# Kernel tuning notes

Hardware: AMD Instinct MI355X
Metric: run time of the kernel (lower is better)

## Reference

```python
import jax, jax.numpy as jnp
import numpy as np

# DeltaNet single-token decode step. Hard-coded dims from the torch source:
# hidden H=2048 (chosen), qk=2048 (16h x 128 -> repeat to 32h), v=4096 (32h x 128),
# conv channels 8192, kernel 4, state [1,32,128,128].
H = 2048
EPS = 1e-6

def _l2norm(x):
    return x * jax.lax.rsqrt(jnp.sum(x * x, axis=-1, keepdims=True) + EPS)

def setup_inputs() -> dict:
    key = jax.random.key(0)
    ks = jax.random.split(key, 12)
    w = lambda k, s, sc=0.02: jax.random.normal(k, s, dtype=jnp.float32) * sc
    return {
        "x": jax.random.normal(ks[0], (1, 1, H), dtype=jnp.float32),
        "state": jax.random.normal(ks[1], (1, 32, 128, 128), dtype=jnp.float32) * 0.02,
        "conv_state": jax.random.normal(ks[2], (1, 8192, 3), dtype=jnp.float32) * 0.1,
        "W_qkv": w(ks[3], (8192, H)),
        "W_z": w(ks[4], (4096, H)),
        "W_b": w(ks[5], (32, H)),
        "W_a": w(ks[6], (32, H)),
        "conv_w": w(ks[7], (8192, 1, 4), 0.3),
        "A_log": jax.random.uniform(ks[8], (32,), minval=-2.0, maxval=0.0, dtype=jnp.float32),
        "dt_bias": w(ks[9], (32,), 0.5),
        "norm_w": jnp.ones((128,), jnp.float32),
        "W_out": w(ks[10], (H, 4096)),
    }

def reference(x, state, conv_state, W_qkv, W_z, W_b, W_a, conv_w, A_log, dt_bias, norm_w, W_out):
    # projections (bias-free Linear, torch convention y = x @ W.T)
    mixed = jnp.einsum('blh,ch->blc', x, W_qkv)           # [1,1,8192]
    z = jnp.einsum('blh,ch->blc', x, W_z).reshape(1, 1, 32, 128)
    beta = jax.nn.sigmoid(jnp.einsum('blh,ch->blc', x, W_b))  # [1,1,32]
    a = jnp.einsum('blh,ch->blc', x, W_a)                 # [1,1,32]

    # depthwise causal conv (groups=8192, kernel 4, output length 1)
    combined = jnp.concatenate([conv_state, mixed.transpose(0, 2, 1)], axis=-1)  # [1,8192,4]
    new_conv = combined[:, :, -3:]
    conv_out = jnp.sum(combined * conv_w[None, :, 0, :], axis=-1)  # [1,8192]
    mixed = jax.nn.silu(conv_out)[:, None, :]             # [1,1,8192]

    q, k, v = mixed[..., :2048], mixed[..., 2048:4096], mixed[..., 4096:]
    q = jnp.repeat(q.reshape(1, 1, 16, 128), 2, axis=2)   # [1,1,32,128]
    k = jnp.repeat(k.reshape(1, 1, 16, 128), 2, axis=2)
    v = v.reshape(1, 1, 32, 128)

    g = -jnp.exp(A_log) * jax.nn.softplus(a + dt_bias)    # [1,1,32]

    q = _l2norm(q)[:, 0] / jnp.sqrt(jnp.float32(128.0))   # [1,32,128]
    k = _l2norm(k)[:, 0]
    v = v[:, 0]
    g_t = jnp.exp(g[:, 0])[..., None, None]               # [1,32,1,1]
    beta_t = beta[:, 0][..., None]                        # [1,32,1]

    # gated delta-rule state update
    s = state * g_t                                       # [1,32,128,128]
    kv_mem = jnp.einsum('bhkv,bhk->bhv', s, k)            # [1,32,128]
    delta = (v - kv_mem) * beta_t
    new_state = s + k[..., None] * delta[..., None, :]    # [1,32,128,128]
    out = jnp.einsum('bhkv,bhk->bhv', new_state, q)       # [1,32,128]

    # gated RMSNorm (Mamba2-style: rmsnorm(x * silu(z)) * w)
    out_flat = out.reshape(-1, 128)
    z_flat = z.reshape(-1, 128)
    gated = out_flat * jax.nn.silu(z_flat)
    out_flat = gated * jax.lax.rsqrt(jnp.mean(gated * gated, axis=-1, keepdims=True) + EPS) * norm_w

    out = jnp.einsum('blc,hc->blh', out_flat.reshape(1, 1, 4096), W_out)  # [1,1,H]
    return (out, new_state, new_conv)
```

## Files before the change

kernel.cpp:

```cpp
#include <hip/hip_runtime.h>
#include <hip/hip_cooperative_groups.h>
#include <math.h>

namespace cg = cooperative_groups;

__device__ __forceinline__ float silu(float x){ return x / (1.f + expf(-x)); }

__device__ __forceinline__ void gemv_in_pairs(
    int pairIdx, int pairStride, int lane,
    const float* __restrict__ x,
    const float* __restrict__ W_qkv, const float* __restrict__ W_z,
    const float* __restrict__ W_b,   const float* __restrict__ W_a,
    float* __restrict__ mixed, float* __restrict__ zb,
    float* __restrict__ b_raw, float* __restrict__ a_raw)
{
  float4 xr[8];
  #pragma unroll
  for (int j = 0; j < 8; j++)
    xr[j] = *(const float4*)(x + j*256 + lane*4);

  for (int rp = pairIdx; rp < 6176; rp += pairStride){
    const int row0 = rp * 2;
    const float* W; float* dst;
    if (row0 < 8192)       { W = W_qkv + (size_t)row0 * 2048;          dst = mixed + row0; }
    else if (row0 < 12288) { W = W_z   + (size_t)(row0-8192) * 2048;   dst = zb + (row0-8192); }
    else if (row0 < 12320) { W = W_b   + (size_t)(row0-12288) * 2048;  dst = b_raw + (row0-12288); }
    else                   { W = W_a   + (size_t)(row0-12320) * 2048;  dst = a_raw + (row0-12320); }

    float acc0 = 0.f, acc1 = 0.f;
    #pragma unroll
    for (int j = 0; j < 8; j++){
      float4 w0 = *(const float4*)(W + j*256 + lane*4);
      float4 w1 = *(const float4*)(W + 2048 + j*256 + lane*4);
      acc0 += w0.x*xr[j].x + w0.y*xr[j].y + w0.z*xr[j].z + w0.w*xr[j].w;
      acc1 += w1.x*xr[j].x + w1.y*xr[j].y + w1.z*xr[j].z + w1.w*xr[j].w;
    }
    #pragma unroll
    for (int off = 32; off >= 1; off >>= 1){
      acc0 += __shfl_xor(acc0, off, 64);
      acc1 += __shfl_xor(acc1, off, 64);
    }
    if (lane == 0){ dst[0] = acc0; dst[1] = acc1; }
  }
}

struct HeadSmem {
  float qn[128];
  float kn[128];
  __align__(16) float vs[128];
  float4 kvp[8][32];
  float red[4];
};

__device__ __forceinline__ void head_work(
    int h, int tid, HeadSmem& sm,
    const float* __restrict__ mixed,      const float* __restrict__ conv_state,
    const float* __restrict__ conv_w,     const float* __restrict__ zbuf,
    const float* __restrict__ b_raw,      const float* __restrict__ a_raw,
    const float* __restrict__ A_log,      const float* __restrict__ dt_bias,
    const float* __restrict__ norm_w,     const float* __restrict__ state,
    float* __restrict__ new_state, float* __restrict__ new_conv,
    float* __restrict__ out_flat)
{
  const int hb = h >> 1;
  const int t  = tid & 127;
  const int lane = tid & 63, wid = tid >> 6;

  float qv = 0.f, kv = 0.f;
  if (tid < 128){
    int c = hb*128 + t;
    float c0 = conv_state[c*3+0], c1 = conv_state[c*3+1], c2 = conv_state[c*3+2];
    float m  = mixed[c];
    qv = silu(c0*conv_w[c*4+0] + c1*conv_w[c*4+1] + c2*conv_w[c*4+2] + m*conv_w[c*4+3]);
    new_conv[c*3+0] = c1; new_conv[c*3+1] = c2; new_conv[c*3+2] = m;
    c = 2048 + hb*128 + t;
    c0 = conv_state[c*3+0]; c1 = conv_state[c*3+1]; c2 = conv_state[c*3+2];
    m  = mixed[c];
    kv = silu(c0*conv_w[c*4+0] + c1*conv_w[c*4+1] + c2*conv_w[c*4+2] + m*conv_w[c*4+3]);
    new_conv[c*3+0] = c1; new_conv[c*3+1] = c2; new_conv[c*3+2] = m;

    float sq = qv*qv, sk = kv*kv;
    #pragma unroll
    for (int off = 32; off >= 1; off >>= 1){
      sq += __shfl_xor(sq, off, 64);
      sk += __shfl_xor(sk, off, 64);
    }
    if (lane == 0){ sm.red[wid] = sq; sm.red[2+wid] = sk; }
  } else {
    int c = 4096 + h*128 + t;
    float c0 = conv_state[c*3+0], c1 = conv_state[c*3+1], c2 = conv_state[c*3+2];
    float m  = mixed[c];
    sm.vs[t] = silu(c0*conv_w[c*4+0] + c1*conv_w[c*4+1] + c2*conv_w[c*4+2] + m*conv_w[c*4+3]);
    new_conv[c*3+0] = c1; new_conv[c*3+1] = c2; new_conv[c*3+2] = m;
  }
  __syncthreads();
  const float qscale = rsqrtf(sm.red[0]+sm.red[1] + 1e-6f) * 0.088388347648318440550f;
  const float kscale = rsqrtf(sm.red[2]+sm.red[3] + 1e-6f);
  if (tid < 128){ sm.qn[t] = qv * qscale; sm.kn[t] = kv * kscale; }
  __syncthreads();

  float g_t, beta;
  {
    const float av = a_raw[h] + dt_bias[h];
    const float sp = (av > 20.f) ? av : log1pf(expf(av));
    g_t  = expf(-expf(A_log[h]) * sp);
    beta = 1.f / (1.f + expf(-b_raw[h]));
  }

  const int cg_ = tid & 31, part = tid >> 5;
  const int k0 = part * 16;
  const float* st  = state     + (size_t)h * 16384;
  float*       nst = new_state + (size_t)h * 16384;

  float4 s4[16];
  float4 kvm = make_float4(0.f, 0.f, 0.f, 0.f);
  #pragma unroll
  for (int i = 0; i < 16; i++){
    float4 sv = *(const float4*)(st + (k0+i)*128 + cg_*4);
    sv.x *= g_t; sv.y *= g_t; sv.z *= g_t; sv.w *= g_t;
    s4[i] = sv;
    const float kk = sm.kn[k0+i];
    kvm.x += sv.x*kk; kvm.y += sv.y*kk; kvm.z += sv.z*kk; kvm.w += sv.w*kk;
  }
  sm.kvp[part][cg_] = kvm;
  __syncthreads();
  float4 kt = make_float4(0.f, 0.f, 0.f, 0.f);
  #pragma unroll
  for (int p = 0; p < 8; p++){
    float4 kp = sm.kvp[p][cg_];
    kt.x += kp.x; kt.y += kp.y; kt.z += kp.z; kt.w += kp.w;
  }
  const float4 v4 = *(const float4*)(sm.vs + cg_*4);
  float4 delta;
  delta.x = (v4.x - kt.x) * beta;
  delta.y = (v4.y - kt.y) * beta;
  delta.z = (v4.z - kt.z) * beta;
  delta.w = (v4.w - kt.w) * beta;

  float4 oacc = make_float4(0.f, 0.f, 0.f, 0.f);
  #pragma unroll
  for (int i = 0; i < 16; i++){
    const float kk = sm.kn[k0+i];
    float4 ns;
    ns.x = s4[i].x + kk*delta.x;
    ns.y = s4[i].y + kk*delta.y;
    ns.z = s4[i].z + kk*delta.z;
    ns.w = s4[i].w + kk*delta.w;
    *(float4*)(nst + (k0+i)*128 + cg_*4) = ns;
    const float qq = sm.qn[k0+i];
    oacc.x += ns.x*qq; oacc.y += ns.y*qq; oacc.z += ns.z*qq; oacc.w += ns.w*qq;
  }
  __syncthreads();
  sm.kvp[part][cg_] = oacc;
  __syncthreads();
  if (part == 0){
    float4 o = make_float4(0.f, 0.f, 0.f, 0.f);
    #pragma unroll
    for (int p = 0; p < 8; p++){
      float4 op = sm.kvp[p][cg_];
      o.x += op.x; o.y += op.y; o.z += op.z; o.w += op.w;
    }
    const float4 z4 = *(const float4*)(zbuf + h*128 + cg_*4);
    float4 g4;
    g4.x = o.x * silu(z4.x);
    g4.y = o.y * silu(z4.y);
    g4.z = o.z * silu(z4.z);
    g4.w = o.w * silu(z4.w);
    float s2 = g4.x*g4.x + g4.y*g4.y + g4.z*g4.z + g4.w*g4.w;
    #pragma unroll
    for (int off = 16; off >= 1; off >>= 1) s2 += __shfl_xor(s2, off, 64);
    const float r = rsqrtf(s2 * (1.f/128.f) + 1e-6f);
    const float4 nw = *(const float4*)(norm_w + cg_*4);
    float4 ov;
    ov.x = g4.x * r * nw.x;
    ov.y = g4.y * r * nw.y;
    ov.z = g4.z * r * nw.z;
    ov.w = g4.w * r * nw.w;
    *(float4*)(out_flat + h*128 + cg_*4) = ov;
  }
}

__global__ __launch_bounds__(256, 4) void k_fused(
    const float* __restrict__ x,
    const float* __restrict__ conv_state,
    const float* __restrict__ W_qkv,
    const float* __restrict__ W_z,
    const float* __restrict__ W_b,
    const float* __restrict__ W_a,
    const float* __restrict__ conv_w,
    const float* __restrict__ A_log,
    const float* __restrict__ dt_bias,
    const float* __restrict__ norm_w,
    const float* __restrict__ state,
    const float* __restrict__ Wout,
    float* __restrict__ out,
    float* __restrict__ new_state,
    float* __restrict__ new_conv,
    float* __restrict__ mixed,
    float* __restrict__ zb,
    float* __restrict__ b_raw,
    float* __restrict__ a_raw,
    float* __restrict__ oflat)
{
  cg::grid_group grid = cg::this_grid();
  const int b    = blockIdx.x;
  const int tid  = threadIdx.x;
  const int lane = tid & 63;
  const int wave = tid >> 6;

  __shared__ HeadSmem sm;
  __shared__ float redC[4];

  gemv_in_pairs(b*4 + wave, 4096, lane, x, W_qkv, W_z, W_b, W_a,
                mixed, zb, b_raw, a_raw);

  grid.sync();

  const int rowC = b*2 + (wave >> 1);
  const int half = wave & 1;
  const float* Wr = Wout + (size_t)rowC * 4096 + half * 2048;

  float4 wreg[8];
  if (b < 32){
    head_work(b, tid, sm, mixed, conv_state, conv_w, zb, b_raw, a_raw,
              A_log, dt_bias, norm_w, state, new_state, new_conv, oflat);
    #pragma unroll
    for (int j = 0; j < 8; j++)
      wreg[j] = *(const float4*)(Wr + j*256 + lane*4);
  } else {
    #pragma unroll
    for (int j = 0; j < 8; j++)
      wreg[j] = *(const float4*)(Wr + j*256 + lane*4);
  }

  grid.sync();

  {
    const float* xh = oflat + half * 2048;
    float acc = 0.f;
    #pragma unroll
    for (int j = 0; j < 8; j++){
      float4 xv = *(const float4*)(xh + j*256 + lane*4);
      acc += wreg[j].x*xv.x + wreg[j].y*xv.y + wreg[j].z*xv.z + wreg[j].w*xv.w;
    }
    #pragma unroll
    for (int off = 32; off >= 1; off >>= 1) acc += __shfl_xor(acc, off, 64);
    if (lane == 0) redC[wave] = acc;
    __syncthreads();
    if (tid < 2) out[b*2 + tid] = redC[2*tid] + redC[2*tid+1];
  }
}

__global__ __launch_bounds__(256) void k_gemv_in(
    const float* __restrict__ x,
    const float* __restrict__ W_qkv, const float* __restrict__ W_z,
    const float* __restrict__ W_b,   const float* __restrict__ W_a,
    float* __restrict__ mixed, float* __restrict__ zb,
    float* __restrict__ b_raw, float* __restrict__ a_raw)
{
  const int lane = threadIdx.x & 63, wave = threadIdx.x >> 6;
  gemv_in_pairs(blockIdx.x*4 + wave, 6176, lane, x, W_qkv, W_z, W_b, W_a,
                mixed, zb, b_raw, a_raw);
}

__global__ __launch_bounds__(256) void k_head(
    const float* __restrict__ mixed,      const float* __restrict__ conv_state,
    const float* __restrict__ conv_w,     const float* __restrict__ zbuf,
    const float* __restrict__ b_raw,      const float* __restrict__ a_raw,
    const float* __restrict__ A_log,      const float* __restrict__ dt_bias,
    const float* __restrict__ norm_w,     const float* __restrict__ state,
    const float* __restrict__ Wout,
    float* __restrict__ new_state, float* __restrict__ new_conv,
    float* __restrict__ out_flat,  float* __restrict__ scratch)
{
  const int b = blockIdx.x, tid = threadIdx.x;
  if (b >= 32){
    const float4* W4 = (const float4*)Wout + (size_t)b * 8192;
    float4 a = make_float4(0.f, 0.f, 0.f, 0.f);
    #pragma unroll
    for (int j = 0; j < 32; j++){
      float4 w = W4[j*256 + tid];
      a.x += w.x; a.y += w.y; a.z += w.z; a.w += w.w;
    }
    if (tid == 0) scratch[b] = a.x + a.y + a.z + a.w;
    return;
  }
  __shared__ HeadSmem sm;
  head_work(b, tid, sm, mixed, conv_state, conv_w, zbuf, b_raw, a_raw,
            A_log, dt_bias, norm_w, state, new_state, new_conv, out_flat);
}

__global__ __launch_bounds__(256) void k_gemv_out(
    const float* __restrict__ out_flat,
    const float* __restrict__ Wout,
    float* __restrict__ out)
{
  __shared__ __align__(16) float xs[4096];
  const int tid = threadIdx.x;
  #pragma unroll
  for (int i = 0; i < 4; i++)
    *(float4*)(xs + tid*4 + i*1024) = *(const float4*)(out_flat + tid*4 + i*1024);
  __syncthreads();

  const int lane = tid & 63, wave = tid >> 6;
  const int row0 = blockIdx.x * 8 + wave * 2;
  const float* W0 = Wout + (size_t)row0 * 4096;
  float acc0 = 0.f, acc1 = 0.f;
  #pragma unroll
  for (int j = 0; j < 16; j++){
    float4 w0 = *(const float4*)(W0 + j*256 + lane*4);
    float4 w1 = *(const float4*)(W0 + 4096 + j*256 + lane*4);
    const float x0 = xs[j*256+lane*4+0], x1 = xs[j*256+lane*4+1];
    const float x2 = xs[j*256+lane*4+2], x3 = xs[j*256+lane*4+3];
    acc0 += w0.x*x0 + w0.y*x1 + w0.z*x2 + w0.w*x3;
    acc1 += w1.x*x0 + w1.y*x1 + w1.z*x2 + w1.w*x3;
  }
  #pragma unroll
  for (int off = 32; off >= 1; off >>= 1){
    acc0 += __shfl_xor(acc0, off, 64);
    acc1 += __shfl_xor(acc1, off, 64);
  }
  if (lane == 0){ out[row0] = acc0; out[row0+1] = acc1; }
}

extern "C" void kernel_launch(void* const* d_in, const int* in_sizes, int n_in,
                              void* d_out, int out_size, void* d_ws, size_t ws_size,
                              hipStream_t stream) {
  const float* x          = (const float*)d_in[0];
  const float* state      = (const float*)d_in[1];
  const float* conv_state = (const float*)d_in[2];
  const float* W_qkv      = (const float*)d_in[3];
  const float* W_z        = (const float*)d_in[4];
  const float* W_b        = (const float*)d_in[5];
  const float* W_a        = (const float*)d_in[6];
  const float* conv_w     = (const float*)d_in[7];
  const float* A_log      = (const float*)d_in[8];
  const float* dt_bias    = (const float*)d_in[9];
  const float* norm_w     = (const float*)d_in[10];
  const float* W_out      = (const float*)d_in[11];

  float* out       = (float*)d_out;
  float* new_state = (float*)d_out + 2048;
  float* new_conv  = (float*)d_out + 2048 + 524288;

  float* ws      = (float*)d_ws;
  float* mixed   = ws;
  float* zb      = ws + 8192;
  float* b_raw   = ws + 12288;
  float* a_raw   = ws + 12320;
  float* oflat   = ws + 12352;
  float* scratch = ws + 16448;

  int maxBlk = 0;
  hipError_t qe = hipOccupancyMaxActiveBlocksPerMultiprocessor(
      &maxBlk, (const void*)k_fused, 256, 0);
  bool coop_ok = (qe == hipSuccess && maxBlk >= 4);

  if (coop_ok){
    void* args[] = {
      (void*)&x, (void*)&conv_state, (void*)&W_qkv, (void*)&W_z, (void*)&W_b,
      (void*)&W_a, (void*)&conv_w, (void*)&A_log, (void*)&dt_bias, (void*)&norm_w,
      (void*)&state, (void*)&W_out,
      (void*)&out, (void*)&new_state, (void*)&new_conv,
      (void*)&mixed, (void*)&zb, (void*)&b_raw, (void*)&a_raw, (void*)&oflat
    };
    hipError_t le = hipLaunchCooperativeKernel((const void*)k_fused,
                                               dim3(1024), dim3(256),
                                               args, 0, stream);
    if (le == hipSuccess) return;
  }

  hipLaunchKernelGGL(k_gemv_in, dim3(1544), dim3(256), 0, stream,
                     x, W_qkv, W_z, W_b, W_a, mixed, zb, b_raw, a_raw);
  hipLaunchKernelGGL(k_head, dim3(256), dim3(256), 0, stream,
                     mixed, conv_state, conv_w, zb, b_raw, a_raw, A_log, dt_bias,
                     norm_w, state, W_out, new_state, new_conv, oflat, scratch);
  hipLaunchKernelGGL(k_gemv_out, dim3(256), dim3(256), 0, stream,
                     oflat, W_out, out);
}
```

Baseline: 177.6 us.

## Replace cooperative grid syncs with targeted atomic-counter barriers

Swaps the two full grid.sync barriers for atomic counters. Only the 32 head blocks wait for all blocks to finish the input GEMV, and all blocks then wait only for those 32 head blocks before the output GEMV. This lets non-head blocks skip the first barrier and keep prefetching W_out while the head work runs. It adds a memset launch to reset the counters each call, and correctness relies on relaxed atomics plus threadfences.

```diff
diff --git a/kernel.cpp b/kernel.cpp
--- a/kernel.cpp
+++ b/kernel.cpp
@@ -1,8 +1,6 @@
 #include <hip/hip_runtime.h>
 #include <hip/hip_cooperative_groups.h>
 #include <math.h>
-
-namespace cg = cooperative_groups;
 
 __device__ __forceinline__ float silu(float x){ return x / (1.f + expf(-x)); }
 
@@ -200,9 +198,10 @@
     float* __restrict__ zb,
     float* __restrict__ b_raw,
     float* __restrict__ a_raw,
-    float* __restrict__ oflat)
-{
-  cg::grid_group grid = cg::this_grid();
+    float* __restrict__ oflat,
+    unsigned int* __restrict__ c1,
+    unsigned int* __restrict__ c2)
+{
   const int b    = blockIdx.x;
   const int tid  = threadIdx.x;
   const int lane = tid & 63;
@@ -213,17 +212,31 @@
 
   gemv_in_pairs(b*4 + wave, 4096, lane, x, W_qkv, W_z, W_b, W_a,
                 mixed, zb, b_raw, a_raw);
-
-  grid.sync();
+  __syncthreads();
+  if (tid == 0){
+    __threadfence();
+    __hip_atomic_fetch_add(c1, 1u, __ATOMIC_RELAXED, __HIP_MEMORY_SCOPE_AGENT);
+  }
 
   const int rowC = b*2 + (wave >> 1);
   const int half = wave & 1;
   const float* Wr = Wout + (size_t)rowC * 4096 + half * 2048;
-
   float4 wreg[8];
+
   if (b < 32){
+    if (tid == 0){
+      while (__hip_atomic_load(c1, __ATOMIC_RELAXED, __HIP_MEMORY_SCOPE_AGENT) < 1024u)
+        __builtin_amdgcn_s_sleep(2);
+      __threadfence();
+    }
+    __syncthreads();
     head_work(b, tid, sm, mixed, conv_state, conv_w, zb, b_raw, a_raw,
               A_log, dt_bias, norm_w, state, new_state, new_conv, oflat);
+    __syncthreads();
+    if (tid == 0){
+      __threadfence();
+      __hip_atomic_fetch_add(c2, 1u, __ATOMIC_RELAXED, __HIP_MEMORY_SCOPE_AGENT);
+    }
     #pragma unroll
     for (int j = 0; j < 8; j++)
       wreg[j] = *(const float4*)(Wr + j*256 + lane*4);
@@ -233,7 +246,12 @@
       wreg[j] = *(const float4*)(Wr + j*256 + lane*4);
   }
 
-  grid.sync();
+  if (tid == 0){
+    while (__hip_atomic_load(c2, __ATOMIC_RELAXED, __HIP_MEMORY_SCOPE_AGENT) < 32u)
+      __builtin_amdgcn_s_sleep(2);
+    __threadfence();
+  }
+  __syncthreads();
 
   {
     const float* xh = oflat + half * 2048;
@@ -350,6 +368,8 @@
   float* a_raw   = ws + 12320;
   float* oflat   = ws + 12352;
   float* scratch = ws + 16448;
+  unsigned int* c1 = (unsigned int*)(ws + 20480);
+  unsigned int* c2 = c1 + 1;
 
   int maxBlk = 0;
   hipError_t qe = hipOccupancyMaxActiveBlocksPerMultiprocessor(
@@ -357,17 +377,21 @@
   bool coop_ok = (qe == hipSuccess && maxBlk >= 4);
 
   if (coop_ok){
-    void* args[] = {
-      (void*)&x, (void*)&conv_state, (void*)&W_qkv, (void*)&W_z, (void*)&W_b,
-      (void*)&W_a, (void*)&conv_w, (void*)&A_log, (void*)&dt_bias, (void*)&norm_w,
-      (void*)&state, (void*)&W_out,
-      (void*)&out, (void*)&new_state, (void*)&new_conv,
-      (void*)&mixed, (void*)&zb, (void*)&b_raw, (void*)&a_raw, (void*)&oflat
-    };
-    hipError_t le = hipLaunchCooperativeKernel((const void*)k_fused,
-                                               dim3(1024), dim3(256),
-                                               args, 0, stream);
-    if (le == hipSuccess) return;
+    hipError_t me = hipMemsetAsync((void*)c1, 0, 64, stream);
+    if (me == hipSuccess){
+      void* args[] = {
+        (void*)&x, (void*)&conv_state, (void*)&W_qkv, (void*)&W_z, (void*)&W_b,
+        (void*)&W_a, (void*)&conv_w, (void*)&A_log, (void*)&dt_bias, (void*)&norm_w,
+        (void*)&state, (void*)&W_out,
+        (void*)&out, (void*)&new_state, (void*)&new_conv,
+        (void*)&mixed, (void*)&zb, (void*)&b_raw, (void*)&a_raw, (void*)&oflat,
+        (void*)&c1, (void*)&c2
+      };
+      hipError_t le = hipLaunchCooperativeKernel((const void*)k_fused,
+                                                 dim3(1024), dim3(256),
+                                                 args, 0, stream);
+      if (le == hipSuccess) return;
+    }
   }
 
   hipLaunchKernelGGL(k_gemv_in, dim3(1544), dim3(256), 0, stream,
```

After: 180.6 us. Within noise of the previous version (+1.7%).
